# Optimization experiments

Measured on AMD Instinct MI355X. Metric: run time of the kernel, lower is better.

The kernel has to match this reference:

```python
import jax, jax.numpy as jnp
import numpy as np

N_ITER = 2
BIG = 1e16  # distance assigned to out-of-range superpixel neighbors (zero affinity)


def reference(x, stoken_size):
    B, C, H, W = x.shape
    sh = sw = int(stoken_size)
    nh, nw = H // sh, W // sw
    ns = nh * nw          # num_spixels
    P = H * W             # n_pixel

    pix = x.reshape(B, C, P)  # (B,C,P)
    # initial centroids: adaptive_avg_pool2d == block mean for divisible sizes
    spix = x.reshape(B, C, nh, sh, nw, sw).mean(axis=(3, 5)).reshape(B, C, ns)

    # init label map (nearest interpolation of the ns-label grid to HxW)
    ly = jnp.arange(H) // sh
    lx = jnp.arange(W) // sw
    init_label = (ly[:, None] * nw + lx[None, :]).reshape(-1)  # (P,)

    # 9-neighbor relative superpixel offsets
    rel = jnp.array([-nw - 1, -nw, -nw + 1, -1, 0, 1, nw - 1, nw, nw + 1])
    sidx = init_label[None, :] + rel[:, None]          # (9,P)
    valid = (sidx >= 0) & (sidx < ns)                  # same mask as get_abs_indices
    sidx_c = jnp.clip(sidx, 0, ns - 1)                 # safe gather index
    cols = jnp.broadcast_to(jnp.arange(P)[None, :], (9, P))
    bidx = jnp.broadcast_to(sidx_c[None], (B, 9, P))

    pn = (pix ** 2).sum(axis=1)   # (B,P)
    abs_aff = jnp.zeros((B, ns, P), x.dtype)
    for k in range(N_ITER):
        # pairwise squared distance pixel <-> 9 candidate superpixels
        sn = (spix ** 2).sum(axis=1)                        # (B,ns)
        dots = jnp.einsum('bcs,bcp->bsp', spix, pix)        # (B,ns,P)
        cross = jnp.take_along_axis(dots, bidx, axis=1)     # (B,9,P)
        sng = sn[:, sidx_c]                                 # (B,9,P)
        dist = pn[:, None, :] - 2.0 * cross + sng           # (B,9,P)
        dist = jnp.where(valid[None], dist, jnp.asarray(BIG, x.dtype))
        aff = jax.nn.softmax(-dist, axis=1) * valid[None]   # (B,9,P)
        # dense sparse-scatter: abs_aff[b, sidx[k,p], p] += aff[b,k,p]
        abs_aff = jnp.zeros((B, ns, P), x.dtype).at[:, sidx_c, cols].add(aff)
        if k < N_ITER - 1:
            num = jnp.einsum('bsp,bcp->bcs', abs_aff, pix)             # (B,C,ns)
            spix = num / (abs_aff.sum(axis=2)[:, None, :] + 1e-16)
    # entire ssn_iter runs under torch.no_grad in the original
    return (jax.lax.stop_gradient(abs_aff), ns)


def setup_inputs() -> dict:
    key = jax.random.key(0)
    x = jax.random.normal(key, (4, 64, 256, 256), dtype=jnp.float32)
    return {"x": x, "stoken_size": 16}
```

## Files before the change

kernel.cpp:

```cpp
#include <hip/hip_runtime.h>

#define BB 4
#define CCH 64
#define HH 256
#define WW 256
#define PP (HH*WW)
#define NS 256


__global__ __launch_bounds__(256) void kA_spix_init(const float* __restrict__ x,
                                                    float* __restrict__ spix) {
    int blk = blockIdx.x;
    int i = blk & 15;
    int c = (blk >> 4) & 63;
    int b = blk >> 10;
    int t = threadIdx.x;
    const float* base = x + ((size_t)(b*CCH + c))*PP + (size_t)i*16*WW + t;
    float s = 0.f;
    #pragma unroll
    for (int r = 0; r < 16; ++r) s += base[(size_t)r*WW];
    #pragma unroll
    for (int off = 8; off; off >>= 1) s += __shfl_down(s, off, 16);
    if ((t & 15) == 0) {
        int j = t >> 4;
        spix[((size_t)b*NS + (i*16 + j))*CCH + c] = s * (1.f/256.f);
    }
}

__global__ __launch_bounds__(256, 4) void kF3(const float* __restrict__ x,
                                              const float* __restrict__ spix,
                                              float* __restrict__ partial,
                                              float* __restrict__ wpart) {
    __shared__ float sp[9][64];
    __shared__ float sn[9];
    __shared__ float affL[9][260];
    __shared__ float pixT[32][260];
    __shared__ float red[4][9][33];
    __shared__ float wsum[4][9];

    int blk = blockIdx.x;
    int l = blk & 255, b = blk >> 8;
    int by = l >> 4, bx = l & 15;
    int t = threadIdx.x;
    int lane = t & 63, w = t >> 6;

    for (int idx = t; idx < 9*64; idx += 256) {
        int k = idx >> 6, c = idx & 63;
        int rel = (k/3 - 1)*16 + (k % 3) - 1;
        int s = l + rel;
        float v = 0.f;
        if (s >= 0 && s < NS) v = spix[((size_t)b*NS + s)*CCH + c];
        sp[k][c] = v;
    }
    __syncthreads();
    if (t < 9) {
        float s = 0.f;
        #pragma unroll
        for (int c4 = 0; c4 < 16; ++c4) {
            float4 v = *reinterpret_cast<const float4*>(&sp[t][c4*4]);
            s += v.x*v.x + v.y*v.y + v.z*v.z + v.w*v.w;
        }
        sn[t] = s;
    }
    __syncthreads();

    int ty = t >> 4, tx = t & 15;
    int gp = (by*16 + ty)*WW + bx*16 + tx;
    const float* px = x + (size_t)b*CCH*PP + gp;

    float cross[9];
    #pragma unroll
    for (int k = 0; k < 9; ++k) cross[k] = 0.f;
    float pn = 0.f;
    #pragma unroll
    for (int cc = 0; cc < 16; ++cc) {
        float v0 = px[(size_t)(cc*4+0)*PP];
        float v1 = px[(size_t)(cc*4+1)*PP];
        float v2 = px[(size_t)(cc*4+2)*PP];
        float v3 = px[(size_t)(cc*4+3)*PP];
        pn += v0*v0 + v1*v1 + v2*v2 + v3*v3;
        #pragma unroll
        for (int k = 0; k < 9; ++k) {
            const float4 s = *reinterpret_cast<const float4*>(&sp[k][cc*4]);
            cross[k] += s.x*v0 + s.y*v1 + s.z*v2 + s.w*v3;
        }
    }

    float e[9];
    float m = -1e30f;
    #pragma unroll
    for (int k = 0; k < 9; ++k) {
        int rel = (k/3 - 1)*16 + (k % 3) - 1;
        int s = l + rel;
        bool valid = (s >= 0) && (s < NS);
        float z = -(pn - 2.f*cross[k] + sn[k]);
        e[k] = valid ? z : -3.0e38f;
        if (valid && z > m) m = z;
    }
    float sum = 0.f;
    #pragma unroll
    for (int k = 0; k < 9; ++k) {
        float v = (e[k] > -2.9e38f) ? expf(e[k] - m) : 0.f;
        e[k] = v;
        sum += v;
    }
    float inv = 1.f / sum;
    #pragma unroll
    for (int k = 0; k < 9; ++k) { e[k] *= inv; affL[k][t] = e[k]; }

    #pragma unroll
    for (int k = 0; k < 9; ++k) {
        float v = e[k];
        #pragma unroll
        for (int off = 32; off; off >>= 1) v += __shfl_xor(v, off);
        if (lane == 0) wsum[w][k] = v;
    }
    __syncthreads();
    if (t < 9) {
        wpart[((size_t)b*9 + t)*NS + l] =
            wsum[0][t] + wsum[1][t] + wsum[2][t] + wsum[3][t];
    }

    int cl = t & 31, q = t >> 5;
    #pragma unroll
    for (int half = 0; half < 2; ++half) {
        if (half) __syncthreads();
        #pragma unroll
        for (int ci = 0; ci < 32; ++ci)
            pixT[ci][t] = px[(size_t)(half*32 + ci)*PP];
        __syncthreads();
        float acc[9];
        #pragma unroll
        for (int k = 0; k < 9; ++k) acc[k] = 0.f;
        #pragma unroll
        for (int i4 = 0; i4 < 8; ++i4) {
            int lp4 = q*32 + i4*4;
            const float4 v = *reinterpret_cast<const float4*>(&pixT[cl][lp4]);
            #pragma unroll
            for (int k = 0; k < 9; ++k) {
                const float4 a = *reinterpret_cast<const float4*>(&affL[k][lp4]);
                acc[k] += a.x*v.x + a.y*v.y + a.z*v.z + a.w*v.w;
            }
        }
        #pragma unroll
        for (int k = 0; k < 9; ++k) acc[k] += __shfl_down(acc[k], 32);
        if (lane < 32) {
            #pragma unroll
            for (int k = 0; k < 9; ++k) red[w][k][cl] = acc[k];
        }
        __syncthreads();
        for (int tt = t; tt < 9*32; tt += 256) {
            int k = tt >> 5, c2 = tt & 31;
            float s = red[0][k][c2] + red[1][k][c2] + red[2][k][c2] + red[3][k][c2];
            partial[(((size_t)b*9 + k)*NS + l)*CCH + half*32 + c2] = s;
        }
    }
}

__global__ __launch_bounds__(256) void kD_update(const float* __restrict__ partial,
                                                 const float* __restrict__ wpart,
                                                 float* __restrict__ spix) {
    int gid = blockIdx.x*256 + threadIdx.x;
    int c = gid & 63, s = (gid >> 6) & 255, b = gid >> 14;
    float num = 0.f, den = 0.f;
    #pragma unroll
    for (int k = 0; k < 9; ++k) {
        int rel = (k/3 - 1)*16 + (k%3 - 1);
        int l = s - rel;
        if (l >= 0 && l < NS) {
            num += partial[(((size_t)b*9 + k)*NS + l)*CCH + c];
            den += wpart[((size_t)b*9 + k)*NS + l];
        }
    }
    spix[((size_t)b*NS + s)*CCH + c] = num / (den + 1e-16f);
}

__global__ __launch_bounds__(256) void kBE(const float* __restrict__ x,
                                           const float* __restrict__ spix,
                                           float* __restrict__ out,
                                           int out_size) {
    __shared__ float spw[50][68];
    __shared__ float snw[50];
    __shared__ float affL[9][260];
    int blk = blockIdx.x;
    int y = blk & 255;
    int b = blk >> 8;
    int t = threadIdx.x;
    int ly = y >> 4;
    int base = ly*16 - 17;

    for (int idx = t; idx < 50*CCH; idx += 256) {
        int j = idx >> 6, c = idx & 63;
        int g = base + j;
        float v = 0.f;
        if (g >= 0 && g < NS) v = spix[((size_t)b*NS + g)*CCH + c];
        spw[j][c] = v;
    }
    __syncthreads();
    if (t < 50) {
        float s = 0.f;
        #pragma unroll
        for (int c4 = 0; c4 < 16; ++c4) {
            float4 v = *reinterpret_cast<const float4*>(&spw[t][c4*4]);
            s += v.x*v.x + v.y*v.y + v.z*v.z + v.w*v.w;
        }
        snw[t] = s;
    }
    __syncthreads();

    int p = y*WW + t;
    const float* px = x + (size_t)b*CCH*PP + p;
    int wl = 17 + (t >> 4);
    int nk[9];
    #pragma unroll
    for (int k = 0; k < 9; ++k) nk[k] = wl + (k/3 - 1)*16 + (k%3 - 1);

    float cross[9];
    #pragma unroll
    for (int k = 0; k < 9; ++k) cross[k] = 0.f;
    float pn = 0.f;
    #pragma unroll
    for (int cc = 0; cc < 16; ++cc) {
        float v0 = px[(size_t)(cc*4+0)*PP];
        float v1 = px[(size_t)(cc*4+1)*PP];
        float v2 = px[(size_t)(cc*4+2)*PP];
        float v3 = px[(size_t)(cc*4+3)*PP];
        pn += v0*v0 + v1*v1 + v2*v2 + v3*v3;
        #pragma unroll
        for (int k = 0; k < 9; ++k) {
            const float4 s = *reinterpret_cast<const float4*>(&spw[nk[k]][cc*4]);
            cross[k] += s.x*v0 + s.y*v1 + s.z*v2 + s.w*v3;
        }
    }

    int label = ly*16 + (t >> 4);
    float e[9];
    float m = -1e30f;
    #pragma unroll
    for (int k = 0; k < 9; ++k) {
        int rel = (k/3 - 1)*16 + (k%3 - 1);
        int sidx = label + rel;
        bool valid = (sidx >= 0) && (sidx < NS);
        float z = -(pn - 2.f*cross[k] + snw[nk[k]]);
        e[k] = valid ? z : -3.0e38f;
        if (valid && z > m) m = z;
    }
    float sum = 0.f;
    #pragma unroll
    for (int k = 0; k < 9; ++k) {
        float v = (e[k] > -2.9e38f) ? expf(e[k] - m) : 0.f;
        e[k] = v;
        sum += v;
    }
    float inv = 1.f / sum;
    #pragma unroll
    for (int k = 0; k < 9; ++k) affL[k][t] = e[k] * inv;
    __syncthreads();

    int w = t >> 6, lane = t & 63;
    int px4 = lane * 4;
    int labelbase = ly*16 + (px4 >> 4);
    float* orow = out + (size_t)b*NS*PP + (size_t)y*WW + px4;
    #pragma unroll 8
    for (int r = 0; r < 64; ++r) {
        int s = w + 4*r;
        int diff = s - labelbase + 17;
        float4 v = make_float4(0.f, 0.f, 0.f, 0.f);
        if ((unsigned)diff <= 34u && (diff & 15) < 3) {
            int k = (diff >> 4)*3 + (diff & 15);
            v = *(const float4*)&affL[k][px4];
        }
        *(float4*)(orow + (size_t)s*PP) = v;
    }
    if (blk == 0 && t == 0) out[out_size - 1] = 256.0f;
}

extern "C" void kernel_launch(void* const* d_in, const int* in_sizes, int n_in,
                              void* d_out, int out_size, void* d_ws, size_t ws_size,
                              hipStream_t stream) {
    (void)in_sizes; (void)n_in; (void)ws_size;
    const float* x = (const float*)d_in[0];
    float* out = (float*)d_out;
    float* ws = (float*)d_ws;

    float* spix    = ws;
    float* partial = spix + (size_t)BB*NS*CCH;
    float* wpart   = partial + (size_t)BB*9*NS*CCH;

    kA_spix_init<<<BB*CCH*16, 256, 0, stream>>>(x, spix);
    kF3<<<BB*NS, 256, 0, stream>>>(x, spix, partial, wpart);
    kD_update<<<BB*NS*CCH/256, 256, 0, stream>>>(partial, wpart, spix);
    kBE<<<BB*HH, 256, 0, stream>>>(x, spix, out, out_size);
}
```

Baseline: 126.1 us.

## Fuse centroid init with transpose of input into superpixel-tiled layout

The first kernel now also writes a copy of the input rearranged so each 16x16 superpixel tile's pixels are contiguous per channel, and the assignment/accumulation kernel reads from this tiled copy instead of strided rows of the original image. The goal is fully contiguous, coalesced 1KB reads per channel in the main kernel, replacing 64-byte row segments. The cost is an extra 64MB write plus a later re-read through the workspace, and the launch-bounds occupancy hint on the main kernel is dropped.

```diff
diff --git a/kernel.cpp b/kernel.cpp
--- a/kernel.cpp
+++ b/kernel.cpp
@@ -8,29 +8,46 @@
 #define NS 256
 
 
-__global__ __launch_bounds__(256) void kA_spix_init(const float* __restrict__ x,
-                                                    float* __restrict__ spix) {
+__global__ __launch_bounds__(256) void kT(const float* __restrict__ x,
+                                          float* __restrict__ xTile,
+                                          float* __restrict__ spix) {
+    __shared__ float lds[16][257];
     int blk = blockIdx.x;
-    int i = blk & 15;
-    int c = (blk >> 4) & 63;
-    int b = blk >> 10;
-    int t = threadIdx.x;
-    const float* base = x + ((size_t)(b*CCH + c))*PP + (size_t)i*16*WW + t;
-    float s = 0.f;
-    #pragma unroll
-    for (int r = 0; r < 16; ++r) s += base[(size_t)r*WW];
-    #pragma unroll
-    for (int off = 8; off; off >>= 1) s += __shfl_down(s, off, 16);
+    int ly = blk & 15;
+    int c  = (blk >> 4) & 63;
+    int b  = blk >> 10;
+    int t  = threadIdx.x;
+
+    const float* src = x + ((size_t)(b*CCH + c))*PP + (size_t)(ly*16)*WW + t;
+    float v[16];
+    #pragma unroll
+    for (int r = 0; r < 16; ++r) v[r] = src[(size_t)r*WW];
+
+    float cs = 0.f;
+    #pragma unroll
+    for (int r = 0; r < 16; ++r) cs += v[r];
+    #pragma unroll
+    for (int off = 8; off; off >>= 1) cs += __shfl_down(cs, off, 16);
     if ((t & 15) == 0) {
-        int j = t >> 4;
-        spix[((size_t)b*NS + (i*16 + j))*CCH + c] = s * (1.f/256.f);
-    }
-}
-
-__global__ __launch_bounds__(256, 4) void kF3(const float* __restrict__ x,
-                                              const float* __restrict__ spix,
-                                              float* __restrict__ partial,
-                                              float* __restrict__ wpart) {
+        int lx = t >> 4;
+        spix[((size_t)b*NS + (ly*16 + lx))*CCH + c] = cs * (1.f/256.f);
+    }
+
+    #pragma unroll
+    for (int r = 0; r < 16; ++r) lds[r][t] = v[r];
+    __syncthreads();
+
+    int r2 = t >> 4, cx = t & 15;
+    float* dst = xTile + (((size_t)(b*NS + ly*16))*CCH + c)*256 + t;
+    #pragma unroll
+    for (int lx = 0; lx < 16; ++lx)
+        dst[(size_t)lx*CCH*256] = lds[r2][lx*16 + cx];
+}
+
+__global__ __launch_bounds__(256) void kF4(const float* __restrict__ xTile,
+                                           const float* __restrict__ spix,
+                                           float* __restrict__ partial,
+                                           float* __restrict__ wpart) {
     __shared__ float sp[9][64];
     __shared__ float sn[9];
     __shared__ float affL[9][260];
@@ -40,7 +57,6 @@
 
     int blk = blockIdx.x;
     int l = blk & 255, b = blk >> 8;
-    int by = l >> 4, bx = l & 15;
     int t = threadIdx.x;
     int lane = t & 63, w = t >> 6;
 
@@ -64,9 +80,7 @@
     }
     __syncthreads();
 
-    int ty = t >> 4, tx = t & 15;
-    int gp = (by*16 + ty)*WW + bx*16 + tx;
-    const float* px = x + (size_t)b*CCH*PP + gp;
+    const float* px = xTile + ((size_t)(b*NS + l))*CCH*256 + t;
 
     float cross[9];
     #pragma unroll
@@ -74,10 +88,10 @@
     float pn = 0.f;
     #pragma unroll
     for (int cc = 0; cc < 16; ++cc) {
-        float v0 = px[(size_t)(cc*4+0)*PP];
-        float v1 = px[(size_t)(cc*4+1)*PP];
-        float v2 = px[(size_t)(cc*4+2)*PP];
-        float v3 = px[(size_t)(cc*4+3)*PP];
+        float v0 = px[(size_t)(cc*4+0)*256];
+        float v1 = px[(size_t)(cc*4+1)*256];
+        float v2 = px[(size_t)(cc*4+2)*256];
+        float v3 = px[(size_t)(cc*4+3)*256];
         pn += v0*v0 + v1*v1 + v2*v2 + v3*v3;
         #pragma unroll
         for (int k = 0; k < 9; ++k) {
@@ -127,7 +141,7 @@
         if (half) __syncthreads();
         #pragma unroll
         for (int ci = 0; ci < 32; ++ci)
-            pixT[ci][t] = px[(size_t)(half*32 + ci)*PP];
+            pixT[ci][t] = px[(size_t)(half*32 + ci)*256];
         __syncthreads();
         float acc[9];
         #pragma unroll
@@ -283,12 +297,13 @@
     float* out = (float*)d_out;
     float* ws = (float*)d_ws;
 
-    float* spix    = ws;
+    float* xTile   = ws;
+    float* spix    = xTile + (size_t)BB*NS*CCH*256;
     float* partial = spix + (size_t)BB*NS*CCH;
     float* wpart   = partial + (size_t)BB*9*NS*CCH;
 
-    kA_spix_init<<<BB*CCH*16, 256, 0, stream>>>(x, spix);
-    kF3<<<BB*NS, 256, 0, stream>>>(x, spix, partial, wpart);
+    kT<<<BB*CCH*16, 256, 0, stream>>>(x, xTile, spix);
+    kF4<<<BB*NS, 256, 0, stream>>>(xTile, spix, partial, wpart);
     kD_update<<<BB*NS*CCH/256, 256, 0, stream>>>(partial, wpart, spix);
     kBE<<<BB*HH, 256, 0, stream>>>(x, spix, out, out_size);
 }
```

New measurement: 124.9 us. About the same (-0.9%).

## Split fused affinity/partial kernel into row-wise affinity and channel-split reduction kernels

Applied to the files above, without the earlier changes.

The fused kF3 kernel, which computed affinities per 16x16 superpixel tile and then reduced affinity-weighted pixels through shared memory, is replaced by two kernels. kFdot processes full image rows with coalesced loads and writes the 9-way affinities to a global workspace. kP then reduces affinity times pixel per superpixel row, with each block handling 4 channels and using shuffle reductions instead of shared-memory transposes. This aims for better coalescing and more parallelism, but it adds an extra global write and re-read of the affinities, and x is read once more.

```diff
diff --git a/kernel.cpp b/kernel.cpp
--- a/kernel.cpp
+++ b/kernel.cpp
@@ -27,46 +27,43 @@
     }
 }
 
-__global__ __launch_bounds__(256, 4) void kF3(const float* __restrict__ x,
-                                              const float* __restrict__ spix,
-                                              float* __restrict__ partial,
-                                              float* __restrict__ wpart) {
-    __shared__ float sp[9][64];
-    __shared__ float sn[9];
-    __shared__ float affL[9][260];
-    __shared__ float pixT[32][260];
-    __shared__ float red[4][9][33];
-    __shared__ float wsum[4][9];
-
+__global__ __launch_bounds__(256) void kFdot(const float* __restrict__ x,
+                                             const float* __restrict__ spix,
+                                             float* __restrict__ aff9) {
+    __shared__ float spw[50][68];
+    __shared__ float snw[50];
     int blk = blockIdx.x;
-    int l = blk & 255, b = blk >> 8;
-    int by = l >> 4, bx = l & 15;
+    int y = blk & 255;
+    int b = blk >> 8;
     int t = threadIdx.x;
-    int lane = t & 63, w = t >> 6;
-
-    for (int idx = t; idx < 9*64; idx += 256) {
-        int k = idx >> 6, c = idx & 63;
-        int rel = (k/3 - 1)*16 + (k % 3) - 1;
-        int s = l + rel;
+    int ly = y >> 4;
+    int base = ly*16 - 17;
+
+    for (int idx = t; idx < 50*CCH; idx += 256) {
+        int j = idx >> 6, c = idx & 63;
+        int g = base + j;
         float v = 0.f;
-        if (s >= 0 && s < NS) v = spix[((size_t)b*NS + s)*CCH + c];
-        sp[k][c] = v;
-    }
-    __syncthreads();
-    if (t < 9) {
+        if (g >= 0 && g < NS) v = spix[((size_t)b*NS + g)*CCH + c];
+        spw[j][c] = v;
+    }
+    __syncthreads();
+    if (t < 50) {
         float s = 0.f;
         #pragma unroll
         for (int c4 = 0; c4 < 16; ++c4) {
-            float4 v = *reinterpret_cast<const float4*>(&sp[t][c4*4]);
+            float4 v = *reinterpret_cast<const float4*>(&spw[t][c4*4]);
             s += v.x*v.x + v.y*v.y + v.z*v.z + v.w*v.w;
         }
-        sn[t] = s;
-    }
-    __syncthreads();
-
-    int ty = t >> 4, tx = t & 15;
-    int gp = (by*16 + ty)*WW + bx*16 + tx;
-    const float* px = x + (size_t)b*CCH*PP + gp;
+        snw[t] = s;
+    }
+    __syncthreads();
+
+    int p = y*WW + t;
+    const float* px = x + (size_t)b*CCH*PP + p;
+    int wl = 17 + (t >> 4);
+    int nk[9];
+    #pragma unroll
+    for (int k = 0; k < 9; ++k) nk[k] = wl + (k/3 - 1)*16 + (k%3 - 1);
 
     float cross[9];
     #pragma unroll
@@ -81,19 +78,20 @@
         pn += v0*v0 + v1*v1 + v2*v2 + v3*v3;
         #pragma unroll
         for (int k = 0; k < 9; ++k) {
-            const float4 s = *reinterpret_cast<const float4*>(&sp[k][cc*4]);
+            const float4 s = *reinterpret_cast<const float4*>(&spw[nk[k]][cc*4]);
             cross[k] += s.x*v0 + s.y*v1 + s.z*v2 + s.w*v3;
         }
     }
 
+    int label = ly*16 + (t >> 4);
     float e[9];
     float m = -1e30f;
     #pragma unroll
     for (int k = 0; k < 9; ++k) {
-        int rel = (k/3 - 1)*16 + (k % 3) - 1;
-        int s = l + rel;
-        bool valid = (s >= 0) && (s < NS);
-        float z = -(pn - 2.f*cross[k] + sn[k]);
+        int rel = (k/3 - 1)*16 + (k%3 - 1);
+        int sidx = label + rel;
+        bool valid = (sidx >= 0) && (sidx < NS);
+        float z = -(pn - 2.f*cross[k] + snw[nk[k]]);
         e[k] = valid ? z : -3.0e38f;
         if (valid && z > m) m = z;
     }
@@ -106,53 +104,76 @@
     }
     float inv = 1.f / sum;
     #pragma unroll
-    for (int k = 0; k < 9; ++k) { e[k] *= inv; affL[k][t] = e[k]; }
-
-    #pragma unroll
-    for (int k = 0; k < 9; ++k) {
-        float v = e[k];
-        #pragma unroll
-        for (int off = 32; off; off >>= 1) v += __shfl_xor(v, off);
-        if (lane == 0) wsum[w][k] = v;
-    }
-    __syncthreads();
-    if (t < 9) {
-        wpart[((size_t)b*9 + t)*NS + l] =
-            wsum[0][t] + wsum[1][t] + wsum[2][t] + wsum[3][t];
-    }
-
-    int cl = t & 31, q = t >> 5;
-    #pragma unroll
-    for (int half = 0; half < 2; ++half) {
-        if (half) __syncthreads();
-        #pragma unroll
-        for (int ci = 0; ci < 32; ++ci)
-            pixT[ci][t] = px[(size_t)(half*32 + ci)*PP];
-        __syncthreads();
-        float acc[9];
-        #pragma unroll
-        for (int k = 0; k < 9; ++k) acc[k] = 0.f;
-        #pragma unroll
-        for (int i4 = 0; i4 < 8; ++i4) {
-            int lp4 = q*32 + i4*4;
-            const float4 v = *reinterpret_cast<const float4*>(&pixT[cl][lp4]);
+    for (int k = 0; k < 9; ++k)
+        aff9[((size_t)b*9 + k)*PP + p] = e[k] * inv;
+}
+
+__global__ __launch_bounds__(256) void kP(const float* __restrict__ x,
+                                          const float* __restrict__ aff9,
+                                          float* __restrict__ partial,
+                                          float* __restrict__ wpart) {
+    int blk = blockIdx.x;
+    int cq = blk & 15, ly = (blk >> 4) & 15, b = blk >> 8;
+    int t = threadIdx.x;
+    int c0 = cq*4;
+    const float* xb = x + (size_t)b*CCH*PP;
+    const float* ab = aff9 + (size_t)b*9*PP;
+
+    float acc[9][4];
+    #pragma unroll
+    for (int k = 0; k < 9; ++k)
+        #pragma unroll
+        for (int dc = 0; dc < 4; ++dc) acc[k][dc] = 0.f;
+    float accw[9];
+    #pragma unroll
+    for (int k = 0; k < 9; ++k) accw[k] = 0.f;
+
+    #pragma unroll 4
+    for (int r = 0; r < 16; ++r) {
+        int p = (ly*16 + r)*WW + t;
+        float a[9];
+        #pragma unroll
+        for (int k = 0; k < 9; ++k) a[k] = ab[(size_t)k*PP + p];
+        #pragma unroll
+        for (int k = 0; k < 9; ++k) accw[k] += a[k];
+        #pragma unroll
+        for (int dc = 0; dc < 4; ++dc) {
+            float xv = xb[(size_t)(c0 + dc)*PP + p];
             #pragma unroll
-            for (int k = 0; k < 9; ++k) {
-                const float4 a = *reinterpret_cast<const float4*>(&affL[k][lp4]);
-                acc[k] += a.x*v.x + a.y*v.y + a.z*v.z + a.w*v.w;
-            }
-        }
-        #pragma unroll
-        for (int k = 0; k < 9; ++k) acc[k] += __shfl_down(acc[k], 32);
-        if (lane < 32) {
+            for (int k = 0; k < 9; ++k) acc[k][dc] += a[k]*xv;
+        }
+    }
+
+    #pragma unroll
+    for (int k = 0; k < 9; ++k) {
+        #pragma unroll
+        for (int dc = 0; dc < 4; ++dc) {
+            float v = acc[k][dc];
+            v += __shfl_down(v, 8, 16);
+            v += __shfl_down(v, 4, 16);
+            v += __shfl_down(v, 2, 16);
+            v += __shfl_down(v, 1, 16);
+            acc[k][dc] = v;
+        }
+    }
+    if ((t & 15) == 0) {
+        int l = ly*16 + (t >> 4);
+        #pragma unroll
+        for (int k = 0; k < 9; ++k)
             #pragma unroll
-            for (int k = 0; k < 9; ++k) red[w][k][cl] = acc[k];
-        }
-        __syncthreads();
-        for (int tt = t; tt < 9*32; tt += 256) {
-            int k = tt >> 5, c2 = tt & 31;
-            float s = red[0][k][c2] + red[1][k][c2] + red[2][k][c2] + red[3][k][c2];
-            partial[(((size_t)b*9 + k)*NS + l)*CCH + half*32 + c2] = s;
+            for (int dc = 0; dc < 4; ++dc)
+                partial[(((size_t)b*9 + k)*NS + l)*CCH + c0 + dc] = acc[k][dc];
+    }
+    if (cq == 0) {
+        #pragma unroll
+        for (int k = 0; k < 9; ++k) {
+            float v = accw[k];
+            v += __shfl_down(v, 8, 16);
+            v += __shfl_down(v, 4, 16);
+            v += __shfl_down(v, 2, 16);
+            v += __shfl_down(v, 1, 16);
+            if ((t & 15) == 0)
+                wpart[((size_t)b*9 + k)*NS + (ly*16 + (t >> 4))] = v;
         }
     }
 }
@@ -284,11 +305,13 @@
     float* ws = (float*)d_ws;
 
     float* spix    = ws;
-    float* partial = spix + (size_t)BB*NS*CCH;
+    float* aff9    = spix + (size_t)BB*NS*CCH;
+    float* partial = aff9 + (size_t)BB*9*PP;
     float* wpart   = partial + (size_t)BB*9*NS*CCH;
 
     kA_spix_init<<<BB*CCH*16, 256, 0, stream>>>(x, spix);
-    kF3<<<BB*NS, 256, 0, stream>>>(x, spix, partial, wpart);
+    kFdot<<<BB*HH, 256, 0, stream>>>(x, spix, aff9);
+    kP<<<BB*16*16, 256, 0, stream>>>(x, aff9, partial, wpart);
     kD_update<<<BB*NS*CCH/256, 256, 0, stream>>>(partial, wpart, spix);
     kBE<<<BB*HH, 256, 0, stream>>>(x, spix, out, out_size);
 }
```

After: 128.6 us. No clear change (+2.0%).
